# Kernel tuning notes

Measured on AMD Instinct MI355X. Metric: run time of the kernel, lower is better.

Reference implementation:

```python
import jax, jax.numpy as jnp
import numpy as np

B, S, D, H, R, N, RK = 2, 2048, 1024, 16, 64, 32, 128
DH = D // H
EPS = 1e-5


def setup_inputs() -> dict:
    key = jax.random.key(0)
    ks = jax.random.split(key, 24)
    f = lambda i, shape, sc=1.0: jax.random.normal(ks[i], shape, dtype=jnp.float32) * sc
    sm = lambda i, shape: jax.nn.softmax(f(i, shape), axis=-1)
    return {
        'x': f(0, (B, S, D)),
        'f_qk': f(1, (N, D, R), 0.02), 'f_v': f(2, (N, D, R), 0.02),
        'r_qk': f(3, (N, R, D), 0.02), 'r_v': f(4, (N, R, D), 0.02),
        'f_know': f(5, (N, D, RK), 0.02), 'r_know': f(6, (N, RK, D), 0.02),
        'W_O': f(7, (D, D), 0.02),
        'gamma1': jnp.ones(D, jnp.float32), 'beta1': jnp.zeros(D, jnp.float32),
        'gamma2': jnp.ones(D, jnp.float32), 'beta2': jnp.zeros(D, jnp.float32),
        'w_fq': sm(8, (B, S, N)), 'w_fk': sm(9, (B, S, N)), 'w_fv': sm(10, (B, S, N)),
        'w_rq': sm(11, (B, S, N)), 'w_rk': sm(12, (B, S, N)), 'w_rv': sm(13, (B, S, N)),
        'w_know_f': sm(14, (B, S, N)), 'w_know_r': sm(15, (B, S, N)),
    }


def _ln(x, g, b):
    mu = jnp.mean(x, axis=-1, keepdims=True)
    var = jnp.mean(jnp.square(x - mu), axis=-1, keepdims=True)
    return g * (x - mu) * jax.lax.rsqrt(var + EPS) + b


def _feature(x, neurons, w):
    # x [B,S,D], neurons [N,D,R], w [B,S,N] -> [B,S,R]
    all_h = jnp.einsum('bsd,ndr->bsnr', x, neurons)
    return jnp.einsum('bsnr,bsn->bsr', all_h, w)


def _restore(h, neurons, w):
    # h [B,S,R], neurons [N,R,D], w [B,S,N] -> [B,S,D]
    # fuse: avoid materializing [B,S,N,D]; outer-product [B,S,N,R] is small
    t = w[..., None] * h[:, :, None, :]
    return jnp.einsum('bsnr,nrd->bsd', t, neurons)


def _causal_attn(Q, K, V):
    # Q,K,V: [B,H,S,DH]
    scale = 1.0 / jnp.sqrt(jnp.asarray(DH, Q.dtype))
    scores = jnp.einsum('bhqd,bhkd->bhqk', Q, K) * scale
    mask = jnp.tril(jnp.ones((S, S), bool))
    scores = jnp.where(mask, scores, jnp.asarray(-jnp.inf, scores.dtype))
    probs = jax.nn.softmax(scores, axis=-1)
    return jnp.einsum('bhqk,bhkd->bhqd', probs, V)


def reference(x, f_qk, f_v, r_qk, r_v, f_know, r_know, W_O,
              gamma1, beta1, gamma2, beta2,
              w_fq, w_fk, w_fv, w_rq, w_rk, w_rv, w_know_f, w_know_r):
    # --- attention circuit ---
    nx = _ln(x, gamma1, beta1)
    h_q = _feature(nx, f_qk, w_fq)
    h_k = _feature(nx, f_qk, w_fk)
    h_v = _feature(nx, f_v, w_fv)
    Q = _restore(h_q, r_qk, w_rq)
    K = _restore(h_k, r_qk, w_rk)
    V = _restore(h_v, r_v, w_rv)
    to_heads = lambda t: t.reshape(B, S, H, DH).transpose(0, 2, 1, 3)
    attn = _causal_attn(to_heads(Q), to_heads(K), to_heads(V))
    attn = attn.transpose(0, 2, 1, 3).reshape(B, S, D)
    attn_out = attn @ W_O.T  # nn.Linear(d_model, d_model, bias=False)
    x = x + attn_out
    # --- knowledge circuit ---
    nx2 = _ln(x, gamma2, beta2)
    h = _feature(nx2, f_know, w_know_f)
    know_out = _restore(h, r_know, w_know_r)
    x = x + know_out
    return x
```

## Files before the change

### kernel.cpp

```cpp
#include <hip/hip_runtime.h>
#include <stdint.h>


typedef __bf16 bf16x8 __attribute__((ext_vector_type(8)));
typedef float f32x4 __attribute__((ext_vector_type(4)));

__device__ __forceinline__ unsigned short f2b(float f) {
  union { float f; unsigned u; } v; v.f = f;
  unsigned u = v.u;
  unsigned r = (u + 0x7FFFu + ((u >> 16) & 1u)) >> 16;
  return (unsigned short)r;
}
__device__ __forceinline__ float b2f(unsigned short h) {
  union { unsigned u; float f; } v; v.u = ((unsigned)h) << 16;
  return v.f;
}
__device__ __forceinline__ unsigned pk2(float lo, float hi) {
  return (unsigned)f2b(lo) | ((unsigned)f2b(hi) << 16);
}
__device__ __forceinline__ unsigned pkt(float lo, float hi) {
  union { float f; unsigned u; } a, b; a.f = lo; b.f = hi;
  return __builtin_amdgcn_perm(b.u, a.u, 0x07060302u);
}

__global__ __launch_bounds__(256) void gemm_bt(
    const unsigned short* __restrict__ A, const unsigned short* __restrict__ Bt,
    void* __restrict__ out, int M, int N, int K) {
  __shared__ unsigned short lsA[128 * 64];
  __shared__ unsigned short lsB[128 * 64];
  const int tid = threadIdx.x;
  const int w = tid >> 6, lane = tid & 63;
  const int quad = lane >> 4, l16 = lane & 15;
  const int wr = w >> 1, wc = w & 1;
  const int row0 = blockIdx.y * 128;
  const int col0 = blockIdx.x * 128;

  const int srow = w * 32 + (lane >> 3);
  const int scg = ((lane & 7) ^ (lane >> 3)) * 8;
  const unsigned short* ap = A + (size_t)(row0 + srow) * K + scg;
  const unsigned short* bp = Bt + (size_t)(col0 + srow) * K + scg;

  const f32x4 fz = {0.f, 0.f, 0.f, 0.f};
  f32x4 acc[4][4];
#pragma unroll
  for (int i = 0; i < 4; ++i)
#pragma unroll
    for (int j = 0; j < 4; ++j) acc[i][j] = fz;

  for (int k0 = 0; k0 < K; k0 += 64) {
#pragma unroll
    for (int i = 0; i < 4; ++i) {
      __builtin_amdgcn_global_load_lds(
          (const __attribute__((address_space(1))) unsigned int*)(ap + (size_t)i * 8 * K + k0),
          (__attribute__((address_space(3))) unsigned int*)&lsA[(w * 32 + i * 8) * 64],
          16, 0, 0);
      __builtin_amdgcn_global_load_lds(
          (const __attribute__((address_space(1))) unsigned int*)(bp + (size_t)i * 8 * K + k0),
          (__attribute__((address_space(3))) unsigned int*)&lsB[(w * 32 + i * 8) * 64],
          16, 0, 0);
    }
    __syncthreads();
#pragma unroll
    for (int kk = 0; kk < 2; ++kk) {
      bf16x8 af[4], bfr[4];
      const int sl = (((kk * 4 + quad) ^ (l16 & 7)) * 8);
#pragma unroll
      for (int mt = 0; mt < 4; ++mt)
        af[mt] = *(const bf16x8*)&lsA[(wr * 64 + mt * 16 + l16) * 64 + sl];
#pragma unroll
      for (int nt = 0; nt < 4; ++nt)
        bfr[nt] = *(const bf16x8*)&lsB[(wc * 64 + nt * 16 + l16) * 64 + sl];
#pragma unroll
      for (int mt = 0; mt < 4; ++mt)
#pragma unroll
        for (int nt = 0; nt < 4; ++nt)
          acc[mt][nt] = __builtin_amdgcn_mfma_f32_16x16x32_bf16(af[mt], bfr[nt], acc[mt][nt], 0, 0, 0);
    }
    __syncthreads();
  }

  const int rb = row0 + wr * 64;
  const int cb = col0 + wc * 64;
#pragma unroll
  for (int mt = 0; mt < 4; ++mt) {
#pragma unroll
    for (int nt = 0; nt < 4; ++nt) {
      const int r = rb + mt * 16 + quad * 4;
      const int c = cb + nt * 16 + l16;
#pragma unroll
      for (int i = 0; i < 4; ++i)
        ((unsigned short*)out)[(size_t)(r + i) * N + c] = f2b(acc[mt][nt][i]);
    }
  }
}

__global__ __launch_bounds__(256) void gemm_qkv2(
    const unsigned short* __restrict__ t_qk, const unsigned short* __restrict__ t_v,
    const unsigned short* __restrict__ r_qkT, const unsigned short* __restrict__ r_vT,
    unsigned short* __restrict__ pQK0, unsigned short* __restrict__ pQK1,
    unsigned short* __restrict__ VT) {
  __shared__ unsigned short lsA[128 * 64];
  __shared__ unsigned short lsB[128 * 64];
  const int K = 2048;
  const int bid = blockIdx.x;
  const unsigned short* A;
  const unsigned short* Bt;
  int row0, col0, kbeg, kend, kind;
  if (bid < 256) {
    const int xcd = bid & 7, j = bid >> 3;
    row0 = (xcd * 4 + (j >> 3)) * 128;
    col0 = (j & 7) * 128;
    A = t_v; Bt = r_vT; kbeg = 0; kend = K; kind = 0;
  } else {
    const int u = bid - 256;
    const int xcd = u & 7, j = u >> 3;
    const int row_l = j >> 4, rem = j & 15;
    const int ks = rem >> 3, col = rem & 7;
    row0 = (xcd * 8 + row_l) * 128;
    col0 = col * 128;
    A = t_qk; Bt = r_qkT; kbeg = ks * 1024; kend = kbeg + 1024; kind = 1 + ks;
  }
  const int tid = threadIdx.x;
  const int w = tid >> 6, lane = tid & 63;
  const int quad = lane >> 4, l16 = lane & 15;
  const int wr = w >> 1, wc = w & 1;

  const int srow = w * 32 + (lane >> 3);
  const int scg = ((lane & 7) ^ (lane >> 3)) * 8;
  const unsigned short* ap = A + (size_t)(row0 + srow) * K + scg;
  const unsigned short* bp = Bt + (size_t)(col0 + srow) * K + scg;

  const f32x4 fz = {0.f, 0.f, 0.f, 0.f};
  f32x4 acc[4][4];
#pragma unroll
  for (int i = 0; i < 4; ++i)
#pragma unroll
    for (int jj = 0; jj < 4; ++jj) acc[i][jj] = fz;

  for (int k0 = kbeg; k0 < kend; k0 += 64) {
#pragma unroll
    for (int i = 0; i < 4; ++i) {
      __builtin_amdgcn_global_load_lds(
          (const __attribute__((address_space(1))) unsigned int*)(ap + (size_t)i * 8 * K + k0),
          (__attribute__((address_space(3))) unsigned int*)&lsA[(w * 32 + i * 8) * 64],
          16, 0, 0);
      __builtin_amdgcn_global_load_lds(
          (const __attribute__((address_space(1))) unsigned int*)(bp + (size_t)i * 8 * K + k0),
          (__attribute__((address_space(3))) unsigned int*)&lsB[(w * 32 + i * 8) * 64],
          16, 0, 0);
    }
    __syncthreads();
#pragma unroll
    for (int kk = 0; kk < 2; ++kk) {
      bf16x8 af[4], bfr[4];
      const int sl = (((kk * 4 + quad) ^ (l16 & 7)) * 8);
#pragma unroll
      for (int mt = 0; mt < 4; ++mt)
        af[mt] = *(const bf16x8*)&lsA[(wr * 64 + mt * 16 + l16) * 64 + sl];
#pragma unroll
      for (int nt = 0; nt < 4; ++nt)
        bfr[nt] = *(const bf16x8*)&lsB[(wc * 64 + nt * 16 + l16) * 64 + sl];
#pragma unroll
      for (int mt = 0; mt < 4; ++mt)
#pragma unroll
        for (int nt = 0; nt < 4; ++nt)
          acc[mt][nt] = __builtin_amdgcn_mfma_f32_16x16x32_bf16(af[mt], bfr[nt], acc[mt][nt], 0, 0, 0);
    }
    __syncthreads();
  }

  const int rb = row0 + wr * 64;
  const int cb = col0 + wc * 64;
  unsigned short* pout = (kind == 1) ? pQK0 : pQK1;
#pragma unroll
  for (int mt = 0; mt < 4; ++mt) {
#pragma unroll
    for (int nt = 0; nt < 4; ++nt) {
      const int r = rb + mt * 16 + quad * 4;
      const int c = cb + nt * 16 + l16;
#pragma unroll
      for (int i = 0; i < 4; ++i) {
        const float v = acc[mt][nt][i];
        if (kind == 0) VT[(size_t)c * 4096 + (r + i)] = f2b(v);
        else pout[(size_t)(r + i) * 1024 + c] = f2b(v);
      }
    }
  }
}

__global__ __launch_bounds__(256) void reduce_qk(
    const unsigned short* __restrict__ p0, const unsigned short* __restrict__ p1,
    unsigned short* __restrict__ out) {
  const int i = (blockIdx.x * 256 + threadIdx.x) * 8;
  uint4 a = *(const uint4*)&p0[i];
  uint4 b = *(const uint4*)&p1[i];
  unsigned r[4];
  const unsigned* aa = (const unsigned*)&a;
  const unsigned* bb = (const unsigned*)&b;
#pragma unroll
  for (int k = 0; k < 4; ++k) {
    const float lo = b2f((unsigned short)(aa[k] & 0xFFFF)) + b2f((unsigned short)(bb[k] & 0xFFFF));
    const float hi = b2f((unsigned short)(aa[k] >> 16)) + b2f((unsigned short)(bb[k] >> 16));
    r[k] = pk2(lo, hi);
  }
  *(uint4*)&out[i] = *(uint4*)r;
}

__global__ __launch_bounds__(256) void gemm_ks4(
    const unsigned short* __restrict__ A, const unsigned short* __restrict__ Bt,
    float* __restrict__ p0, float* __restrict__ p1,
    float* __restrict__ p2, float* __restrict__ p3, int K) {
  __shared__ unsigned short lsA[128 * 64];
  __shared__ unsigned short lsB[128 * 64];
  const int N = 1024;
  const int bid = blockIdx.x;
  const int xcd = bid & 7, j = bid >> 3;
  const int row_l = j >> 5, rem = j & 31;
  const int ks = rem >> 3, col = rem & 7;
  const int row0 = (xcd * 4 + row_l) * 128;
  const int col0 = col * 128;
  const int kq = K >> 2;
  const int kbeg = ks * kq, kend = kbeg + kq;
  const int tid = threadIdx.x;
  const int w = tid >> 6, lane = tid & 63;
  const int quad = lane >> 4, l16 = lane & 15;
  const int wr = w >> 1, wc = w & 1;

  const int srow = w * 32 + (lane >> 3);
  const int scg = ((lane & 7) ^ (lane >> 3)) * 8;
  const unsigned short* ap = A + (size_t)(row0 + srow) * K + scg;
  const unsigned short* bp = Bt + (size_t)(col0 + srow) * K + scg;

  const f32x4 fz = {0.f, 0.f, 0.f, 0.f};
  f32x4 acc[4][4];
#pragma unroll
  for (int i = 0; i < 4; ++i)
#pragma unroll
    for (int jj = 0; jj < 4; ++jj) acc[i][jj] = fz;

  for (int k0 = kbeg; k0 < kend; k0 += 64) {
#pragma unroll
    for (int i = 0; i < 4; ++i) {
      __builtin_amdgcn_global_load_lds(
          (const __attribute__((address_space(1))) unsigned int*)(ap + (size_t)i * 8 * K + k0),
          (__attribute__((address_space(3))) unsigned int*)&lsA[(w * 32 + i * 8) * 64],
          16, 0, 0);
      __builtin_amdgcn_global_load_lds(
          (const __attribute__((address_space(1))) unsigned int*)(bp + (size_t)i * 8 * K + k0),
          (__attribute__((address_space(3))) unsigned int*)&lsB[(w * 32 + i * 8) * 64],
          16, 0, 0);
    }
    __syncthreads();
#pragma unroll
    for (int kk = 0; kk < 2; ++kk) {
      bf16x8 af[4], bfr[4];
      const int sl = (((kk * 4 + quad) ^ (l16 & 7)) * 8);
#pragma unroll
      for (int mt = 0; mt < 4; ++mt)
        af[mt] = *(const bf16x8*)&lsA[(wr * 64 + mt * 16 + l16) * 64 + sl];
#pragma unroll
      for (int nt = 0; nt < 4; ++nt)
        bfr[nt] = *(const bf16x8*)&lsB[(wc * 64 + nt * 16 + l16) * 64 + sl];
#pragma unroll
      for (int mt = 0; mt < 4; ++mt)
#pragma unroll
        for (int nt = 0; nt < 4; ++nt)
          acc[mt][nt] = __builtin_amdgcn_mfma_f32_16x16x32_bf16(af[mt], bfr[nt], acc[mt][nt], 0, 0, 0);
    }
    __syncthreads();
  }

  float* out = (ks == 0) ? p0 : (ks == 1) ? p1 : (ks == 2) ? p2 : p3;
  const int rb = row0 + wr * 64;
  const int cb = col0 + wc * 64;
#pragma unroll
  for (int mt = 0; mt < 4; ++mt) {
#pragma unroll
    for (int nt = 0; nt < 4; ++nt) {
      const int r = rb + mt * 16 + quad * 4;
      const int c = cb + nt * 16 + l16;
#pragma unroll
      for (int i = 0; i < 4; ++i)
        out[(size_t)(r + i) * N + c] = acc[mt][nt][i];
    }
  }
}

__global__ __launch_bounds__(256) void reduce_add5(
    const float* __restrict__ p0, const float* __restrict__ p1,
    const float* __restrict__ p2, const float* __restrict__ p3,
    const float* __restrict__ res, float* __restrict__ out) {
  const int i = (blockIdx.x * 256 + threadIdx.x) * 4;
  const f32x4 a = *(const f32x4*)&p0[i];
  const f32x4 b = *(const f32x4*)&p1[i];
  const f32x4 c = *(const f32x4*)&p2[i];
  const f32x4 d = *(const f32x4*)&p3[i];
  const f32x4 e = *(const f32x4*)&res[i];
  f32x4 o;
#pragma unroll
  for (int k = 0; k < 4; ++k) o[k] = ((a[k] + b[k]) + (c[k] + d[k])) + e[k];
  *(f32x4*)&out[i] = o;
}

__global__ __launch_bounds__(256) void ln_kernel(
    const float* __restrict__ x, const float* __restrict__ g,
    const float* __restrict__ be, unsigned short* __restrict__ out) {
  __shared__ float sbuf[4];
  const int t = blockIdx.x, tid = threadIdx.x;
  const float* row = x + (size_t)t * 1024;
  float v[4], s = 0.f;
#pragma unroll
  for (int j = 0; j < 4; ++j) { v[j] = row[tid + j * 256]; s += v[j]; }
#pragma unroll
  for (int off = 32; off; off >>= 1) s += __shfl_xor(s, off);
  if ((tid & 63) == 0) sbuf[tid >> 6] = s;
  __syncthreads();
  const float mu = (sbuf[0] + sbuf[1] + sbuf[2] + sbuf[3]) * (1.f / 1024.f);
  __syncthreads();
  float ss = 0.f;
#pragma unroll
  for (int j = 0; j < 4; ++j) { const float d = v[j] - mu; ss += d * d; }
#pragma unroll
  for (int off = 32; off; off >>= 1) ss += __shfl_xor(ss, off);
  if ((tid & 63) == 0) sbuf[tid >> 6] = ss;
  __syncthreads();
  const float var = (sbuf[0] + sbuf[1] + sbuf[2] + sbuf[3]) * (1.f / 1024.f);
  const float rstd = rsqrtf(var + 1e-5f);
  unsigned short* orow = out + (size_t)t * 1024;
#pragma unroll
  for (int j = 0; j < 4; ++j) {
    const int c = tid + j * 256;
    orow[c] = f2b((v[j] - mu) * rstd * g[c] + be[c]);
  }
}

__global__ __launch_bounds__(256) void mix_attn(
    const unsigned short* __restrict__ all_h,
    const float* __restrict__ w_fq, const float* __restrict__ w_fk,
    const float* __restrict__ w_fv, const float* __restrict__ w_rq,
    const float* __restrict__ w_rk, const float* __restrict__ w_rv,
    unsigned short* __restrict__ t_qk, unsigned short* __restrict__ t_v) {
  __shared__ float hq[64], hk[64], hv[64];
  const int t = blockIdx.x, tid = threadIdx.x;
  const int wv = tid >> 6, lane = tid & 63;
  const unsigned short* row = all_h + (size_t)t * 4096;
  if (wv < 3) {
    const float* wf = (wv == 0 ? w_fq : wv == 1 ? w_fk : w_fv) + (size_t)t * 32;
    const int base = (wv == 2) ? 2048 : 0;
    float acc = 0.f;
#pragma unroll
    for (int n = 0; n < 32; ++n) acc += wf[n] * b2f(row[base + n * 64 + lane]);
    (wv == 0 ? hq : wv == 1 ? hk : hv)[lane] = acc;
  }
  __syncthreads();
  const float* wrq = w_rq + (size_t)t * 32;
  const float* wrk = w_rk + (size_t)t * 32;
  const float* wrv = w_rv + (size_t)t * 32;
  for (int idx = tid; idx < 2048; idx += 256) {
    const int n = idx >> 6, r = idx & 63;
    t_qk[(size_t)t * 2048 + idx] = f2b(wrq[n] * hq[r]);
    t_qk[(size_t)(4096 + t) * 2048 + idx] = f2b(wrk[n] * hk[r]);
    t_v[(size_t)t * 2048 + idx] = f2b(wrv[n] * hv[r]);
  }
}

__global__ __launch_bounds__(256) void mix_know(
    const unsigned short* __restrict__ all_h, const float* __restrict__ w_f,
    const float* __restrict__ w_r, unsigned short* __restrict__ t_know) {
  __shared__ float h[128];
  const int t = blockIdx.x, tid = threadIdx.x;
  const unsigned short* row = all_h + (size_t)t * 4096;
  if (tid < 128) {
    const float* wf = w_f + (size_t)t * 32;
    float acc = 0.f;
#pragma unroll
    for (int n = 0; n < 32; ++n) acc += wf[n] * b2f(row[n * 128 + tid]);
    h[tid] = acc;
  }
  __syncthreads();
  const float* wr = w_r + (size_t)t * 32;
  for (int idx = tid; idx < 4096; idx += 256) {
    const int n = idx >> 7, r = idx & 127;
    t_know[(size_t)t * 4096 + idx] = f2b(wr[n] * h[r]);
  }
}

__global__ __launch_bounds__(256) void prep_all(
    const float* __restrict__ f_qk, const float* __restrict__ f_v,
    const float* __restrict__ f_know, const float* __restrict__ r_qk,
    const float* __restrict__ r_v, const float* __restrict__ r_know,
    const float* __restrict__ W_O,
    unsigned short* __restrict__ fcomb, unsigned short* __restrict__ fknowT,
    unsigned short* __restrict__ r_qkT, unsigned short* __restrict__ r_vT,
    unsigned short* __restrict__ r_knowT, unsigned short* __restrict__ WO_bf) {
  __shared__ float tile[32][33];
  const int bid = blockIdx.x;
  const int tx = threadIdx.x, ty = threadIdx.y;
  const float* in;
  unsigned short* out;
  int R, C, gx, loc;
  if (bid < 2048)       { in = f_qk;   out = fcomb;                         R = 1024; C = 64;   gx = 2;  loc = bid; }
  else if (bid < 4096)  { in = f_v;    out = fcomb + (size_t)2048 * 1024;   R = 1024; C = 64;   gx = 2;  loc = bid - 2048; }
  else if (bid < 8192)  { in = f_know; out = fknowT;                        R = 1024; C = 128;  gx = 4;  loc = bid - 4096; }
  else if (bid < 10240) { in = r_qk;   out = r_qkT;                         R = 2048; C = 1024; gx = 32; loc = bid - 8192; }
  else if (bid < 12288) { in = r_v;    out = r_vT;                          R = 2048; C = 1024; gx = 32; loc = bid - 10240; }
  else if (bid < 16384) { in = r_know; out = r_knowT;                       R = 4096; C = 1024; gx = 32; loc = bid - 12288; }
  else {
    const int i = ((bid - 16384) * 256 + ty * 32 + tx) * 4;
    const f32x4 v = *(const f32x4*)&W_O[i];
    *(unsigned*)&WO_bf[i] = pk2(v[0], v[1]);
    *(unsigned*)&WO_bf[i + 2] = pk2(v[2], v[3]);
    return;
  }
  const int tiles = gx * (R >> 5);
  const int bb = loc / tiles, rem = loc % tiles;
  const int r0 = (rem / gx) * 32, c0 = (rem % gx) * 32;
  const float* ip = in + (size_t)bb * R * C;
  unsigned short* op = out + (size_t)bb * R * C;
#pragma unroll
  for (int j = 0; j < 4; ++j)
    tile[ty + j * 8][tx] = ip[(size_t)(r0 + ty + j * 8) * C + c0 + tx];
  __syncthreads();
#pragma unroll
  for (int j = 0; j < 4; ++j)
    op[(size_t)(c0 + ty + j * 8) * R + r0 + tx] = f2b(tile[tx][ty + j * 8]);
}

__global__ __launch_bounds__(256) void flash_split(
    const unsigned short* __restrict__ Q, const unsigned short* __restrict__ Kp,
    const unsigned short* __restrict__ VT, unsigned short* __restrict__ O,
    float* __restrict__ Opart, float* __restrict__ ml) {
  __shared__ unsigned short Kls[2][64 * 64];
  __shared__ unsigned short Vls[2][64 * 64];
  const int uidx = 79 - (int)blockIdx.x;
  int uu = uidx, qt = 0, ch = 0;
  for (int q = 0; q < 32; ++q) {
    const int n = (q >> 3) + 1;
    if (uu < n) { qt = q; ch = uu; break; }
    uu -= n;
  }
  const int bh = blockIdx.y;
  const int b = bh >> 4, h = bh & 15;
  const int tid = threadIdx.x;
  const int w = tid >> 6, lane = tid & 63, quad = lane >> 4, l16 = lane & 15;
  const int tb = b * 2048;
  const int qrow = qt * 64 + w * 16;
  const int ktlo = ch * 8;
  const int kthi = min(qt, ch * 8 + 7);
  const float C = 0.18033688f;

  const int srow = (lane >> 3);
  const int scol = ((lane & 7) ^ srow) * 8;

  bf16x8 qf[2];
#pragma unroll
  for (int kk = 0; kk < 2; ++kk)
    qf[kk] = *(const bf16x8*)&Q[(size_t)(tb + qrow + l16) * 1024 + h * 64 + kk * 32 + quad * 8];

  const f32x4 fz = {0.f, 0.f, 0.f, 0.f};
  float m_i = -1e30f, l_i = 0.f;
  f32x4 o_acc[4];
#pragma unroll
  for (int nt = 0; nt < 4; ++nt) o_acc[nt] = fz;

  auto stage = [&](int buf, int kt) {
#pragma unroll
    for (int j = 0; j < 2; ++j) {
      const int rg = (w * 2 + j) * 8 + srow;
      __builtin_amdgcn_global_load_lds(
          (const __attribute__((address_space(1))) unsigned int*)
              (Kp + (size_t)(tb + kt * 64 + rg) * 1024 + h * 64 + scol),
          (__attribute__((address_space(3))) unsigned int*)&Kls[buf][(w * 2 + j) * 8 * 64],
          16, 0, 0);
      __builtin_amdgcn_global_load_lds(
          (const __attribute__((address_space(1))) unsigned int*)
              (VT + (size_t)(h * 64 + rg) * 4096 + tb + kt * 64 + scol),
          (__attribute__((address_space(3))) unsigned int*)&Vls[buf][(w * 2 + j) * 8 * 64],
          16, 0, 0);
    }
  };

  const int srcA = (((quad & 1) * 32 + l16) << 2);
  const int srcB = srcA + 64;
  const bool hiq = (quad >= 2);

  stage(0, ktlo);
  __syncthreads();
  int buf = 0;
  for (int kt = ktlo; kt <= kthi; ++kt) {
    bf16x8 kf[8], vf[8];
#pragma unroll
    for (int kk = 0; kk < 2; ++kk)
#pragma unroll
      for (int nt = 0; nt < 4; ++nt) {
        const int sl = (((kk * 4 + quad) ^ (l16 & 7)) * 8);
        kf[kk * 4 + nt] = *(const bf16x8*)&Kls[buf][(nt * 16 + l16) * 64 + sl];
        vf[kk * 4 + nt] = *(const bf16x8*)&Vls[buf][(nt * 16 + l16) * 64 + sl];
      }
    if (kt < kthi) stage(buf ^ 1, kt + 1);

    const bool diag = (kt == qt);
    const int ntmax = diag ? (w + 1) : 4;
    f32x4 s[4];
#pragma unroll
    for (int nt = 0; nt < 4; ++nt) s[nt] = fz;
#pragma unroll
    for (int kk = 0; kk < 2; ++kk)
#pragma unroll
      for (int nt = 0; nt < 4; ++nt)
        if (nt < ntmax)
          s[nt] = __builtin_amdgcn_mfma_f32_16x16x32_bf16(kf[kk * 4 + nt], qf[kk], s[nt], 0, 0, 0);

    const int qloc = w * 16 + l16;
    float mx = -1e30f;
#pragma unroll
    for (int nt = 0; nt < 4; ++nt) {
      if (nt >= ntmax) continue;
#pragma unroll
      for (int i = 0; i < 4; ++i) {
        float v = s[nt][i];
        if (diag && (nt * 16 + quad * 4 + i) > qloc) v = -1e30f;
        s[nt][i] = v;
        mx = fmaxf(mx, v);
      }
    }
    mx = fmaxf(mx, __shfl_xor(mx, 16));
    mx = fmaxf(mx, __shfl_xor(mx, 32));
    const float mn = fmaxf(m_i, mx);
    const float al = exp2f((m_i - mn) * C);
    m_i = mn;
    const float mC = mn * C;
    float rs = 0.f;
#pragma unroll
    for (int nt = 0; nt < 4; ++nt) {
      if (nt >= ntmax) {
#pragma unroll
        for (int i = 0; i < 4; ++i) s[nt][i] = 0.f;
        continue;
      }
#pragma unroll
      for (int i = 0; i < 4; ++i) {
        const float p = exp2f(fmaf(s[nt][i], C, -mC));
        s[nt][i] = p;
        rs += p;
      }
    }
    rs += __shfl_xor(rs, 16);
    rs += __shfl_xor(rs, 32);
    l_i = l_i * al + rs;
#pragma unroll
    for (int nt = 0; nt < 4; ++nt)
#pragma unroll
      for (int i = 0; i < 4; ++i) o_acc[nt][i] *= al;

    unsigned pk[4][2];
#pragma unroll
    for (int nt = 0; nt < 4; ++nt) {
      pk[nt][0] = pkt(s[nt][0], s[nt][1]);
      pk[nt][1] = pkt(s[nt][2], s[nt][3]);
    }
#pragma unroll
    for (int kk = 0; kk < 2; ++kk) {
      const int ea = 2 * kk, eb = 2 * kk + 1;
      const unsigned u0 = __builtin_amdgcn_ds_bpermute(srcA, pk[ea][0]);
      const unsigned u1 = __builtin_amdgcn_ds_bpermute(srcA, pk[ea][1]);
      const unsigned u2 = __builtin_amdgcn_ds_bpermute(srcB, pk[ea][0]);
      const unsigned u3 = __builtin_amdgcn_ds_bpermute(srcB, pk[ea][1]);
      const unsigned w0 = __builtin_amdgcn_ds_bpermute(srcA, pk[eb][0]);
      const unsigned w1 = __builtin_amdgcn_ds_bpermute(srcA, pk[eb][1]);
      const unsigned w2 = __builtin_amdgcn_ds_bpermute(srcB, pk[eb][0]);
      const unsigned w3 = __builtin_amdgcn_ds_bpermute(srcB, pk[eb][1]);
      unsigned dw[4];
      dw[0] = hiq ? w0 : u0;
      dw[1] = hiq ? w1 : u1;
      dw[2] = hiq ? w2 : u2;
      dw[3] = hiq ? w3 : u3;
      const bf16x8 pf = *(const bf16x8*)dw;
#pragma unroll
      for (int nt = 0; nt < 4; ++nt)
        o_acc[nt] = __builtin_amdgcn_mfma_f32_16x16x32_bf16(vf[kk * 4 + nt], pf, o_acc[nt], 0, 0, 0);
    }
    __syncthreads();
    buf ^= 1;
  }

  const int nch = (qt >> 3) + 1;
  if (nch == 1) {
    const float inv = 1.0f / l_i;
    unsigned short* orow = O + (size_t)(tb + qrow + l16) * 1024 + h * 64;
#pragma unroll
    for (int nt = 0; nt < 4; ++nt) {
      const unsigned d0 = pk2(o_acc[nt][0] * inv, o_acc[nt][1] * inv);
      const unsigned d1 = pk2(o_acc[nt][2] * inv, o_acc[nt][3] * inv);
      *(unsigned*)&orow[nt * 16 + quad * 4] = d0;
      *(unsigned*)&orow[nt * 16 + quad * 4 + 2] = d1;
    }
  } else {
    const int slot = bh * 80 + uidx;
    const int lq = w * 16 + l16;
    float* op = Opart + ((size_t)slot * 64 + lq) * 64;
#pragma unroll
    for (int nt = 0; nt < 4; ++nt)
      *(f32x4*)&op[nt * 16 + quad * 4] = o_acc[nt];
    if (quad == 0) {
      ml[(size_t)slot * 128 + lq * 2] = m_i;
      ml[(size_t)slot * 128 + lq * 2 + 1] = l_i;
    }
  }
}

__global__ __launch_bounds__(256) void flash_reduce(
    const float* __restrict__ Opart, const float* __restrict__ ml,
    unsigned short* __restrict__ O) {
  const int qt = 8 + blockIdx.x;
  const int bh = blockIdx.y;
  const int b = bh >> 4, h = bh & 15;
  const int j = qt >> 3;
  const int base = 8 * (j * (j + 1) / 2) + (qt - 8 * j) * (j + 1);
  const int nch = j + 1;
  const int tid = threadIdx.x;
  const int lq = tid >> 2, dq = (tid & 3) * 16;
  const float C = 0.18033688f;

  float mc[4], lc[4];
  float m = -1e30f;
#pragma unroll
  for (int c = 0; c < 4; ++c) {
    if (c < nch) {
      const size_t sl = (size_t)(bh * 80 + base + c) * 128 + lq * 2;
      mc[c] = ml[sl];
      lc[c] = ml[sl + 1];
    } else { mc[c] = -1e30f; lc[c] = 0.f; }
    m = fmaxf(m, mc[c]);
  }
  float fac[4], lt = 0.f;
#pragma unroll
  for (int c = 0; c < 4; ++c) {
    fac[c] = (c < nch) ? exp2f((mc[c] - m) * C) : 0.f;
    lt += fac[c] * lc[c];
  }
  const float inv = 1.0f / lt;
  float acc[16];
#pragma unroll
  for (int i = 0; i < 16; ++i) acc[i] = 0.f;
#pragma unroll
  for (int c = 0; c < 4; ++c) {
    if (c >= nch) continue;
    const float* op = Opart + ((size_t)(bh * 80 + base + c) * 64 + lq) * 64 + dq;
#pragma unroll
    for (int i = 0; i < 16; i += 4) {
      const f32x4 v = *(const f32x4*)&op[i];
#pragma unroll
      for (int k = 0; k < 4; ++k) acc[i + k] += fac[c] * v[k];
    }
  }
  unsigned short* orow = O + (size_t)(b * 2048 + qt * 64 + lq) * 1024 + h * 64 + dq;
#pragma unroll
  for (int i = 0; i < 16; i += 2)
    *(unsigned*)&orow[i] = pk2(acc[i] * inv, acc[i + 1] * inv);
}

extern "C" void kernel_launch(void* const* d_in, const int* in_sizes, int n_in,
                              void* d_out, int out_size, void* d_ws, size_t ws_size,
                              hipStream_t stream) {
  (void)in_sizes; (void)n_in; (void)out_size; (void)ws_size;
  const float* x      = (const float*)d_in[0];
  const float* f_qk   = (const float*)d_in[1];
  const float* f_v    = (const float*)d_in[2];
  const float* r_qk   = (const float*)d_in[3];
  const float* r_v    = (const float*)d_in[4];
  const float* f_know = (const float*)d_in[5];
  const float* r_know = (const float*)d_in[6];
  const float* W_O    = (const float*)d_in[7];
  const float* gamma1 = (const float*)d_in[8];
  const float* beta1  = (const float*)d_in[9];
  const float* gamma2 = (const float*)d_in[10];
  const float* beta2  = (const float*)d_in[11];
  const float* w_fq   = (const float*)d_in[12];
  const float* w_fk   = (const float*)d_in[13];
  const float* w_fv   = (const float*)d_in[14];
  const float* w_rq   = (const float*)d_in[15];
  const float* w_rk   = (const float*)d_in[16];
  const float* w_rv   = (const float*)d_in[17];
  const float* w_kf   = (const float*)d_in[18];
  const float* w_kr   = (const float*)d_in[19];

  char* base = (char*)d_ws;
  size_t off = 0;
  auto alloc = [&](size_t b) { char* p = base + off; off += (b + 255) & ~(size_t)255; return p; };
  unsigned short* fcomb   = (unsigned short*)alloc(8388608);
  unsigned short* fknowT  = (unsigned short*)alloc(8388608);
  unsigned short* r_qkT   = (unsigned short*)alloc(4194304);
  unsigned short* r_vT    = (unsigned short*)alloc(4194304);
  unsigned short* r_knowT = (unsigned short*)alloc(8388608);
  unsigned short* WO_bf   = (unsigned short*)alloc(2097152);
  unsigned short* nx_bf   = (unsigned short*)alloc(8388608);
  unsigned short* all_h   = (unsigned short*)alloc(33554432);
  unsigned short* t_qk    = (unsigned short*)alloc(33554432);
  unsigned short* t_v     = (unsigned short*)alloc(16777216);
  unsigned short* QKbuf   = (unsigned short*)alloc(16777216);
  unsigned short* VT      = (unsigned short*)alloc(8388608);
  unsigned short* attn    = (unsigned short*)alloc(8388608);
  float* x1 = (float*)t_v;
  unsigned short* pQK0 = all_h;
  unsigned short* pQK1 = all_h + 8388608;
  float* Opart = (float*)all_h;
  float* mlbuf = (float*)((char*)all_h + 41943040);
  float* pW0 = (float*)all_h;
  float* pW1 = (float*)((char*)all_h + 16777216);
  float* pW2 = (float*)QKbuf;
  float* pW3_wo   = (float*)t_qk;
  float* pW3_know = (float*)VT;

  const dim3 blk256(256), blkT(32, 8);

  prep_all<<<17408, blkT, 0, stream>>>(f_qk, f_v, f_know, r_qk, r_v, r_know, W_O,
                                       fcomb, fknowT, r_qkT, r_vT, r_knowT, WO_bf);

  ln_kernel<<<4096, blk256, 0, stream>>>(x, gamma1, beta1, nx_bf);
  gemm_bt<<<dim3(32, 32), blk256, 0, stream>>>(nx_bf, fcomb, all_h, 4096, 4096, 1024);
  mix_attn<<<4096, blk256, 0, stream>>>(all_h, w_fq, w_fk, w_fv, w_rq, w_rk, w_rv, t_qk, t_v);
  gemm_qkv2<<<1280, blk256, 0, stream>>>(t_qk, t_v, r_qkT, r_vT, pQK0, pQK1, VT);
  reduce_qk<<<4096, blk256, 0, stream>>>(pQK0, pQK1, QKbuf);
  flash_split<<<dim3(80, 32), blk256, 0, stream>>>(QKbuf, QKbuf + (size_t)4096 * 1024, VT, attn,
                                                   Opart, mlbuf);
  flash_reduce<<<dim3(24, 32), blk256, 0, stream>>>(Opart, mlbuf, attn);
  gemm_ks4<<<1024, blk256, 0, stream>>>(attn, WO_bf, pW0, pW1, pW2, pW3_wo, 1024);
  reduce_add5<<<4096, blk256, 0, stream>>>(pW0, pW1, pW2, pW3_wo, x, x1);

  ln_kernel<<<4096, blk256, 0, stream>>>(x1, gamma2, beta2, nx_bf);
  gemm_bt<<<dim3(32, 32), blk256, 0, stream>>>(nx_bf, fknowT, all_h, 4096, 4096, 1024);
  mix_know<<<4096, blk256, 0, stream>>>(all_h, w_kf, w_kr, t_qk);
  gemm_ks4<<<1024, blk256, 0, stream>>>(t_qk, r_knowT, pW0, pW1, pW2, pW3_know, 4096);
  reduce_add5<<<4096, blk256, 0, stream>>>(pW0, pW1, pW2, pW3_know, x1, (float*)d_out);
}
```

Before: 557.8 us.

## Drop split-K for QK and W_O GEMMs, vectorize mix stores, tune flash softmax

Replaces the split-K QK projection and its reduce kernel with a single full-K GEMM that writes QK directly. Replaces the 4-way split-K W_O GEMM and reduce_add5 with a 128x64-tile GEMM that adds the residual in its epilogue. Vectorizes the mix_attn and mix_know outer-product stores to 16-byte packed writes. In flash attention it skips the rescale when the running max is unchanged, uses per-tile partial max and sum reductions, and raises wave priority around the MFMA blocks. Together these remove launches and partial-sum memory traffic, at the cost of fewer blocks (less parallelism) in the two GEMMs.

```diff
diff --git a/kernel.cpp b/kernel.cpp
--- a/kernel.cpp
+++ b/kernel.cpp
@@ -94,31 +94,28 @@
   }
 }
 
-__global__ __launch_bounds__(256) void gemm_qkv2(
+__global__ __launch_bounds__(256) void gemm_qkv(
     const unsigned short* __restrict__ t_qk, const unsigned short* __restrict__ t_v,
     const unsigned short* __restrict__ r_qkT, const unsigned short* __restrict__ r_vT,
-    unsigned short* __restrict__ pQK0, unsigned short* __restrict__ pQK1,
-    unsigned short* __restrict__ VT) {
+    unsigned short* __restrict__ QK, unsigned short* __restrict__ VT) {
   __shared__ unsigned short lsA[128 * 64];
   __shared__ unsigned short lsB[128 * 64];
   const int K = 2048;
   const int bid = blockIdx.x;
   const unsigned short* A;
   const unsigned short* Bt;
-  int row0, col0, kbeg, kend, kind;
+  int row0, col0, isv;
   if (bid < 256) {
     const int xcd = bid & 7, j = bid >> 3;
     row0 = (xcd * 4 + (j >> 3)) * 128;
     col0 = (j & 7) * 128;
-    A = t_v; Bt = r_vT; kbeg = 0; kend = K; kind = 0;
+    A = t_v; Bt = r_vT; isv = 1;
   } else {
     const int u = bid - 256;
     const int xcd = u & 7, j = u >> 3;
-    const int row_l = j >> 4, rem = j & 15;
-    const int ks = rem >> 3, col = rem & 7;
-    row0 = (xcd * 8 + row_l) * 128;
-    col0 = col * 128;
-    A = t_qk; Bt = r_qkT; kbeg = ks * 1024; kend = kbeg + 1024; kind = 1 + ks;
+    row0 = (xcd * 8 + (j >> 3)) * 128;
+    col0 = (j & 7) * 128;
+    A = t_qk; Bt = r_qkT; isv = 0;
   }
   const int tid = threadIdx.x;
   const int w = tid >> 6, lane = tid & 63;
@@ -137,7 +134,7 @@
 #pragma unroll
     for (int jj = 0; jj < 4; ++jj) acc[i][jj] = fz;
 
-  for (int k0 = kbeg; k0 < kend; k0 += 64) {
+  for (int k0 = 0; k0 < K; k0 += 64) {
 #pragma unroll
     for (int i = 0; i < 4; ++i) {
       __builtin_amdgcn_global_load_lds(
@@ -171,7 +168,6 @@
 
   const int rb = row0 + wr * 64;
   const int cb = col0 + wc * 64;
-  unsigned short* pout = (kind == 1) ? pQK0 : pQK1;
 #pragma unroll
   for (int mt = 0; mt < 4; ++mt) {
 #pragma unroll
@@ -181,29 +177,11 @@
 #pragma unroll
       for (int i = 0; i < 4; ++i) {
         const float v = acc[mt][nt][i];
-        if (kind == 0) VT[(size_t)c * 4096 + (r + i)] = f2b(v);
-        else pout[(size_t)(r + i) * 1024 + c] = f2b(v);
+        if (isv) VT[(size_t)c * 4096 + (r + i)] = f2b(v);
+        else QK[(size_t)(r + i) * 1024 + c] = f2b(v);
       }
     }
   }
-}
-
-__global__ __launch_bounds__(256) void reduce_qk(
-    const unsigned short* __restrict__ p0, const unsigned short* __restrict__ p1,
-    unsigned short* __restrict__ out) {
-  const int i = (blockIdx.x * 256 + threadIdx.x) * 8;
-  uint4 a = *(const uint4*)&p0[i];
-  uint4 b = *(const uint4*)&p1[i];
-  unsigned r[4];
-  const unsigned* aa = (const unsigned*)&a;
-  const unsigned* bb = (const unsigned*)&b;
-#pragma unroll
-  for (int k = 0; k < 4; ++k) {
-    const float lo = b2f((unsigned short)(aa[k] & 0xFFFF)) + b2f((unsigned short)(bb[k] & 0xFFFF));
-    const float hi = b2f((unsigned short)(aa[k] >> 16)) + b2f((unsigned short)(bb[k] >> 16));
-    r[k] = pk2(lo, hi);
-  }
-  *(uint4*)&out[i] = *(uint4*)r;
 }
 
 __global__ __launch_bounds__(256) void gemm_ks4(
@@ -286,6 +264,82 @@
   }
 }
 
+__global__ __launch_bounds__(256) void gemm_wo_res(
+    const unsigned short* __restrict__ A, const unsigned short* __restrict__ Bt,
+    const float* __restrict__ res, float* __restrict__ out) {
+  __shared__ unsigned short lsA[128 * 64];
+  __shared__ unsigned short lsB[64 * 64];
+  const int K = 1024, N = 1024;
+  const int bid = blockIdx.x;
+  const int xcd = bid & 7, j = bid >> 3;
+  const int row0 = (xcd * 4 + (j & 3)) * 128;
+  const int col0 = (j >> 2) * 64;
+  const int tid = threadIdx.x;
+  const int w = tid >> 6, lane = tid & 63;
+  const int quad = lane >> 4, l16 = lane & 15;
+  const int wr = w >> 1, wc = w & 1;
+
+  const int srowA = w * 32 + (lane >> 3);
+  const int srowB = w * 16 + (lane >> 3);
+  const int scg = ((lane & 7) ^ (lane >> 3)) * 8;
+  const unsigned short* ap = A + (size_t)(row0 + srowA) * K + scg;
+  const unsigned short* bp = Bt + (size_t)(col0 + srowB) * K + scg;
+
+  const f32x4 fz = {0.f, 0.f, 0.f, 0.f};
+  f32x4 acc[4][2];
+#pragma unroll
+  for (int i = 0; i < 4; ++i)
+#pragma unroll
+    for (int jj = 0; jj < 2; ++jj) acc[i][jj] = fz;
+
+  for (int k0 = 0; k0 < K; k0 += 64) {
+#pragma unroll
+    for (int i = 0; i < 4; ++i)
+      __builtin_amdgcn_global_load_lds(
+          (const __attribute__((address_space(1))) unsigned int*)(ap + (size_t)i * 8 * K + k0),
+          (__attribute__((address_space(3))) unsigned int*)&lsA[(w * 32 + i * 8) * 64],
+          16, 0, 0);
+#pragma unroll
+    for (int i = 0; i < 2; ++i)
+      __builtin_amdgcn_global_load_lds(
+          (const __attribute__((address_space(1))) unsigned int*)(bp + (size_t)i * 8 * K + k0),
+          (__attribute__((address_space(3))) unsigned int*)&lsB[(w * 16 + i * 8) * 64],
+          16, 0, 0);
+    __syncthreads();
+#pragma unroll
+    for (int kk = 0; kk < 2; ++kk) {
+      bf16x8 af[4], bfr[2];
+      const int sl = (((kk * 4 + quad) ^ (l16 & 7)) * 8);
+#pragma unroll
+      for (int mt = 0; mt < 4; ++mt)
+        af[mt] = *(const bf16x8*)&lsA[(wr * 64 + mt * 16 + l16) * 64 + sl];
+#pragma unroll
+      for (int nt = 0; nt < 2; ++nt)
+        bfr[nt] = *(const bf16x8*)&lsB[(wc * 32 + nt * 16 + l16) * 64 + sl];
+#pragma unroll
+      for (int mt = 0; mt < 4; ++mt)
+#pragma unroll
+        for (int nt = 0; nt < 2; ++nt)
+          acc[mt][nt] = __builtin_amdgcn_mfma_f32_16x16x32_bf16(af[mt], bfr[nt], acc[mt][nt], 0, 0, 0);
+    }
+    __syncthreads();
+  }
+
+  const int rb = row0 + wr * 64;
+  const int cb = col0 + wc * 32;
+#pragma unroll
+  for (int mt = 0; mt < 4; ++mt) {
+#pragma unroll
+    for (int nt = 0; nt < 2; ++nt) {
+      const int r = rb + mt * 16 + quad * 4;
+      const int c = cb + nt * 16 + l16;
+#pragma unroll
+      for (int i = 0; i < 4; ++i)
+        out[(size_t)(r + i) * N + c] = acc[mt][nt][i] + res[(size_t)(r + i) * N + c];
+    }
+  }
+}
+
 __global__ __launch_bounds__(256) void reduce_add5(
     const float* __restrict__ p0, const float* __restrict__ p1,
     const float* __restrict__ p2, const float* __restrict__ p3,
@@ -342,26 +396,31 @@
     unsigned short* __restrict__ t_qk, unsigned short* __restrict__ t_v) {
   __shared__ float hq[64], hk[64], hv[64];
   const int t = blockIdx.x, tid = threadIdx.x;
-  const int wv = tid >> 6, lane = tid & 63;
+  const int wvi = tid >> 6, lane = tid & 63;
   const unsigned short* row = all_h + (size_t)t * 4096;
-  if (wv < 3) {
-    const float* wf = (wv == 0 ? w_fq : wv == 1 ? w_fk : w_fv) + (size_t)t * 32;
-    const int base = (wv == 2) ? 2048 : 0;
+  if (wvi < 3) {
+    const float* wf = (wvi == 0 ? w_fq : wvi == 1 ? w_fk : w_fv) + (size_t)t * 32;
+    const int base = (wvi == 2) ? 2048 : 0;
     float acc = 0.f;
 #pragma unroll
     for (int n = 0; n < 32; ++n) acc += wf[n] * b2f(row[base + n * 64 + lane]);
-    (wv == 0 ? hq : wv == 1 ? hk : hv)[lane] = acc;
+    (wvi == 0 ? hq : wvi == 1 ? hk : hv)[lane] = acc;
   }
   __syncthreads();
-  const float* wrq = w_rq + (size_t)t * 32;
-  const float* wrk = w_rk + (size_t)t * 32;
-  const float* wrv = w_rv + (size_t)t * 32;
-  for (int idx = tid; idx < 2048; idx += 256) {
-    const int n = idx >> 6, r = idx & 63;
-    t_qk[(size_t)t * 2048 + idx] = f2b(wrq[n] * hq[r]);
-    t_qk[(size_t)(4096 + t) * 2048 + idx] = f2b(wrk[n] * hk[r]);
-    t_v[(size_t)t * 2048 + idx] = f2b(wrv[n] * hv[r]);
-  }
+  const int n = tid >> 3, r0 = (tid & 7) * 8;
+  const float wq = w_rq[(size_t)t * 32 + n];
+  const float wk = w_rk[(size_t)t * 32 + n];
+  const float wv2 = w_rv[(size_t)t * 32 + n];
+  unsigned dq[4], dk[4], dv[4];
+#pragma unroll
+  for (int jj = 0; jj < 4; ++jj) {
+    dq[jj] = pk2(wq * hq[r0 + 2 * jj], wq * hq[r0 + 2 * jj + 1]);
+    dk[jj] = pk2(wk * hk[r0 + 2 * jj], wk * hk[r0 + 2 * jj + 1]);
+    dv[jj] = pk2(wv2 * hv[r0 + 2 * jj], wv2 * hv[r0 + 2 * jj + 1]);
+  }
+  *(uint4*)&t_qk[(size_t)t * 2048 + tid * 8] = *(uint4*)dq;
+  *(uint4*)&t_qk[(size_t)(4096 + t) * 2048 + tid * 8] = *(uint4*)dk;
+  *(uint4*)&t_v[(size_t)t * 2048 + tid * 8] = *(uint4*)dv;
 }
 
 __global__ __launch_bounds__(256) void mix_know(
@@ -378,11 +437,14 @@
     h[tid] = acc;
   }
   __syncthreads();
-  const float* wr = w_r + (size_t)t * 32;
-  for (int idx = tid; idx < 4096; idx += 256) {
-    const int n = idx >> 7, r = idx & 127;
-    t_know[(size_t)t * 4096 + idx] = f2b(wr[n] * h[r]);
-  }
+  const int n = tid >> 3, r0 = (tid & 7) * 16;
+  const float wn = w_r[(size_t)t * 32 + n];
+  unsigned d[8];
+#pragma unroll
+  for (int jj = 0; jj < 8; ++jj)
+    d[jj] = pk2(wn * h[r0 + 2 * jj], wn * h[r0 + 2 * jj + 1]);
+  *(uint4*)&t_know[(size_t)t * 4096 + tid * 16] = *(uint4*)d;
+  *(uint4*)&t_know[(size_t)t * 4096 + tid * 16 + 8] = *(uint4*)&d[4];
 }
 
 __global__ __launch_bounds__(256) void prep_all(
@@ -504,15 +566,17 @@
     f32x4 s[4];
 #pragma unroll
     for (int nt = 0; nt < 4; ++nt) s[nt] = fz;
+    __builtin_amdgcn_s_setprio(1);
 #pragma unroll
     for (int kk = 0; kk < 2; ++kk)
 #pragma unroll
       for (int nt = 0; nt < 4; ++nt)
         if (nt < ntmax)
           s[nt] = __builtin_amdgcn_mfma_f32_16x16x32_bf16(kf[kk * 4 + nt], qf[kk], s[nt], 0, 0, 0);
+    __builtin_amdgcn_s_setprio(0);
 
     const int qloc = w * 16 + l16;
-    float mx = -1e30f;
+    float mxs[4] = {-1e30f, -1e30f, -1e30f, -1e30f};
 #pragma unroll
     for (int nt = 0; nt < 4; ++nt) {
       if (nt >= ntmax) continue;
@@ -521,16 +585,24 @@
         float v = s[nt][i];
         if (diag && (nt * 16 + quad * 4 + i) > qloc) v = -1e30f;
         s[nt][i] = v;
-        mx = fmaxf(mx, v);
+        mxs[nt] = fmaxf(mxs[nt], v);
       }
     }
+    float mx = fmaxf(fmaxf(mxs[0], mxs[1]), fmaxf(mxs[2], mxs[3]));
     mx = fmaxf(mx, __shfl_xor(mx, 16));
     mx = fmaxf(mx, __shfl_xor(mx, 32));
-    const float mn = fmaxf(m_i, mx);
-    const float al = exp2f((m_i - mn) * C);
-    m_i = mn;
-    const float mC = mn * C;
-    float rs = 0.f;
+    if (!__all(mx <= m_i)) {
+      const float mn = fmaxf(m_i, mx);
+      const float al = exp2f((m_i - mn) * C);
+      m_i = mn;
+      l_i *= al;
+#pragma unroll
+      for (int nt = 0; nt < 4; ++nt)
+#pragma unroll
+        for (int i = 0; i < 4; ++i) o_acc[nt][i] *= al;
+    }
+    const float mC = m_i * C;
+    float rsv[4] = {0.f, 0.f, 0.f, 0.f};
 #pragma unroll
     for (int nt = 0; nt < 4; ++nt) {
       if (nt >= ntmax) {
@@ -542,16 +614,13 @@
       for (int i = 0; i < 4; ++i) {
         const float p = exp2f(fmaf(s[nt][i], C, -mC));
         s[nt][i] = p;
-        rs += p;
+        rsv[nt] += p;
       }
     }
+    float rs = (rsv[0] + rsv[1]) + (rsv[2] + rsv[3]);
     rs += __shfl_xor(rs, 16);
     rs += __shfl_xor(rs, 32);
-    l_i = l_i * al + rs;
-#pragma unroll
-    for (int nt = 0; nt < 4; ++nt)
-#pragma unroll
-      for (int i = 0; i < 4; ++i) o_acc[nt][i] *= al;
+    l_i += rs;
 
     unsigned pk[4][2];
 #pragma unroll
@@ -576,9 +645,11 @@
       dw[2] = hiq ? w2 : u2;
       dw[3] = hiq ? w3 : u3;
       const bf16x8 pf = *(const bf16x8*)dw;
+      __builtin_amdgcn_s_setprio(1);
 #pragma unroll
       for (int nt = 0; nt < 4; ++nt)
         o_acc[nt] = __builtin_amdgcn_mfma_f32_16x16x32_bf16(vf[kk * 4 + nt], pf, o_acc[nt], 0, 0, 0);
+      __builtin_amdgcn_s_setprio(0);
     }
     __syncthreads();
     buf ^= 1;
@@ -702,14 +773,11 @@
   unsigned short* VT      = (unsigned short*)alloc(8388608);
   unsigned short* attn    = (unsigned short*)alloc(8388608);
   float* x1 = (float*)t_v;
-  unsigned short* pQK0 = all_h;
-  unsigned short* pQK1 = all_h + 8388608;
   float* Opart = (float*)all_h;
   float* mlbuf = (float*)((char*)all_h + 41943040);
   float* pW0 = (float*)all_h;
   float* pW1 = (float*)((char*)all_h + 16777216);
   float* pW2 = (float*)QKbuf;
-  float* pW3_wo   = (float*)t_qk;
   float* pW3_know = (float*)VT;
 
   const dim3 blk256(256), blkT(32, 8);
@@ -720,13 +788,11 @@
   ln_kernel<<<4096, blk256, 0, stream>>>(x, gamma1, beta1, nx_bf);
   gemm_bt<<<dim3(32, 32), blk256, 0, stream>>>(nx_bf, fcomb, all_h, 4096, 4096, 1024);
   mix_attn<<<4096, blk256, 0, stream>>>(all_h, w_fq, w_fk, w_fv, w_rq, w_rk, w_rv, t_qk, t_v);
-  gemm_qkv2<<<1280, blk256, 0, stream>>>(t_qk, t_v, r_qkT, r_vT, pQK0, pQK1, VT);
-  reduce_qk<<<4096, blk256, 0, stream>>>(pQK0, pQK1, QKbuf);
+  gemm_qkv<<<768, blk256, 0, stream>>>(t_qk, t_v, r_qkT, r_vT, QKbuf, VT);
   flash_split<<<dim3(80, 32), blk256, 0, stream>>>(QKbuf, QKbuf + (size_t)4096 * 1024, VT, attn,
                                                    Opart, mlbuf);
   flash_reduce<<<dim3(24, 32), blk256, 0, stream>>>(Opart, mlbuf, attn);
-  gemm_ks4<<<1024, blk256, 0, stream>>>(attn, WO_bf, pW0, pW1, pW2, pW3_wo, 1024);
-  reduce_add5<<<4096, blk256, 0, stream>>>(pW0, pW1, pW2, pW3_wo, x, x1);
+  gemm_wo_res<<<512, blk256, 0, stream>>>(attn, WO_bf, x, x1);
 
   ln_kernel<<<4096, blk256, 0, stream>>>(x1, gamma2, beta2, nx_bf);
   gemm_bt<<<dim3(32, 32), blk256, 0, stream>>>(nx_bf, fknowT, all_h, 4096, 4096, 1024);
```

Result: faster. 531.2 us (-4.8%).
